# Kernel tuning notes

Measured on AMD Instinct MI355X. Metric: run time of the kernel, lower is better.

Reference implementation:

```python
import jax, jax.numpy as jnp
import numpy as np

B, C, H, W = 4, 256, 64, 64
G = 32          # GroupNorm groups
EPS = 1e-6


def setup_inputs() -> dict:
    key = jax.random.key(0)
    ks = jax.random.split(key, 6)
    inp = {
        "x": jax.random.normal(ks[0], (B, C, H, W), dtype=jnp.float32),
        "gamma": jnp.ones((C,), jnp.float32),
        "beta": jnp.zeros((C,), jnp.float32),
        "wq": jax.random.normal(ks[1], (C, C), jnp.float32) * 0.02,
        "bq": jnp.zeros((C,), jnp.float32),
        "wk": jax.random.normal(ks[2], (C, C), jnp.float32) * 0.02,
        "bk": jnp.zeros((C,), jnp.float32),
        "wv": jax.random.normal(ks[3], (C, C), jnp.float32) * 0.02,
        "bv": jnp.zeros((C,), jnp.float32),
        "wp": jax.random.normal(ks[4], (C, C), jnp.float32) * 0.02,
        "bp": jnp.zeros((C,), jnp.float32),
    }
    return inp


def _group_norm(x, gamma, beta):
    b, c, h, w = x.shape
    xs = x.reshape(b, G, c // G, h, w)
    mu = xs.mean(axis=(2, 3, 4), keepdims=True)
    var = xs.var(axis=(2, 3, 4), keepdims=True)  # biased, matches torch GroupNorm
    xn = ((xs - mu) * jax.lax.rsqrt(var + EPS)).reshape(b, c, h, w)
    return xn * gamma[None, :, None, None] + beta[None, :, None, None]


def _conv1x1(s, w, bias):
    # 1x1 conv == per-pixel channel matmul
    return jnp.einsum('oc,bchw->bohw', w, s) + bias[None, :, None, None]


def reference(x, gamma, beta, wq, bq, wk, bk, wv, bv, wp, bp):
    b, c, h, w = x.shape
    s = _group_norm(x, gamma, beta)
    q = _conv1x1(s, wq, bq).reshape(b, c, h * w)  # [B, C, N]
    k = _conv1x1(s, wk, bk).reshape(b, c, h * w)
    v = _conv1x1(s, wv, bv).reshape(b, c, h * w)
    # scores[b,i,j] = sum_c q[b,c,i] k[b,c,j], scaled by C^-1/2
    scores = jnp.einsum('bci,bcj->bij', q, k) * (c ** -0.5)
    attn = jax.nn.softmax(scores, axis=2)
    # h_[b,c,i] = sum_j v[b,c,j] attn[b,i,j]
    h_ = jnp.einsum('bij,bcj->bci', attn, v).reshape(b, c, h, w)
    h_ = _conv1x1(h_, wp, bp)
    return x + h_
```

## Files before the change

### kernel.cpp

```cpp
#include <hip/hip_runtime.h>

#define BB 4
#define CCH 256
#define NPIX 4096
#define EPS 1e-6f

typedef __attribute__((ext_vector_type(8))) short bf16x8;
typedef __attribute__((ext_vector_type(4))) float f32x4;
typedef __attribute__((ext_vector_type(16))) float f32x16;

__device__ __forceinline__ unsigned short f2bf(float f) {
    return (unsigned short)((__float_as_uint(f) + 0x8000u) >> 16);
}
__device__ __forceinline__ float bf2f(unsigned short h) {
    return __uint_as_float((unsigned)h << 16);
}
__device__ __forceinline__ void gl2lds16(const void* g, void* l) {
    __builtin_amdgcn_global_load_lds(
        (const __attribute__((address_space(1))) unsigned int*)g,
        (__attribute__((address_space(3))) unsigned int*)l, 16, 0, 0);
}
__device__ __forceinline__ unsigned int comb2(unsigned int u0, unsigned int u1,
                                              float f) {
    float lo = (bf2f((unsigned short)u0) + bf2f((unsigned short)u1)) * f;
    float hi = (bf2f((unsigned short)(u0 >> 16)) +
                bf2f((unsigned short)(u1 >> 16))) * f;
    return (unsigned int)f2bf(lo) | ((unsigned int)f2bf(hi) << 16);
}

__global__ __launch_bounds__(512) void gn_fused(
    const float* __restrict__ x, const float* __restrict__ gamma,
    const float* __restrict__ beta,
    const float* __restrict__ wq, const float* __restrict__ wk,
    const float* __restrict__ wv, const float* __restrict__ wp,
    unsigned short* __restrict__ sb, unsigned short* __restrict__ wb) {
    int bid = blockIdx.x;
    int t = threadIdx.x;
    if (bid >= 128) {
        int e = (bid - 128) * 512 + t;
        const float* srcs[4] = {wp, wq, wk, wv};
#pragma unroll
        for (int m = 0; m < 4; ++m) {
            float4 v = ((const float4*)srcs[m])[e];
            ushort4 hh;
            hh.x = f2bf(v.x); hh.y = f2bf(v.y);
            hh.z = f2bf(v.z); hh.w = f2bf(v.w);
            *(ushort4*)(wb + (size_t)m * 65536 + (size_t)e * 4) = hh;
        }
        return;
    }
    int b = bid >> 5, g = bid & 31;
    const float4* x4 = (const float4*)(x + (size_t)(b * CCH + g * 8) * NPIX);
    float s = 0.f, ss = 0.f;
    for (int e = t; e < 8192; e += 512) {
        float4 v = x4[e];
        s += v.x + v.y + v.z + v.w;
        ss += v.x * v.x + v.y * v.y + v.z * v.z + v.w * v.w;
    }
#pragma unroll
    for (int off = 1; off < 64; off <<= 1) {
        s += __shfl_xor(s, off);
        ss += __shfl_xor(ss, off);
    }
    __shared__ float ws[8], wss[8];
    int w = t >> 6, lane = t & 63;
    if (lane == 0) { ws[w] = s; wss[w] = ss; }
    __syncthreads();
    float S = 0.f, SS = 0.f;
#pragma unroll
    for (int i = 0; i < 8; ++i) { S += ws[i]; SS += wss[i]; }
    const float inv = 1.0f / (float)(8 * NPIX);
    float m = S * inv;
    float var = SS * inv - m * m;
    float rstd = rsqrtf(var + EPS);
    float scale[8], shift[8];
#pragma unroll
    for (int ci = 0; ci < 8; ++ci) {
        float ga = gamma[g * 8 + ci], be = beta[g * 8 + ci];
        scale[ci] = rstd * ga;
        shift[ci] = be - m * scale[ci];
    }
#pragma unroll 1
    for (int r = 0; r < 2; ++r) {
        int pq = r * 512 + t;
        __align__(16) unsigned short hh[4][8];
#pragma unroll
        for (int ci = 0; ci < 8; ++ci) {
            float4 v = x4[ci * 1024 + pq];
            hh[0][ci] = f2bf(v.x * scale[ci] + shift[ci]);
            hh[1][ci] = f2bf(v.y * scale[ci] + shift[ci]);
            hh[2][ci] = f2bf(v.z * scale[ci] + shift[ci]);
            hh[3][ci] = f2bf(v.w * scale[ci] + shift[ci]);
        }
        size_t base = ((size_t)(b * NPIX + pq * 4) << 8) + g * 8;
#pragma unroll
        for (int p = 0; p < 4; ++p)
            *(uint4*)(sb + base + (size_t)p * 256) = *(const uint4*)hh[p];
    }
}

__global__ __launch_bounds__(256) void qkv_mfma(
    const unsigned short* __restrict__ sb, const unsigned short* __restrict__ wb,
    const float* __restrict__ bq, const float* __restrict__ bk,
    const float* __restrict__ bv,
    unsigned short* __restrict__ qT, unsigned short* __restrict__ kT,
    unsigned short* __restrict__ vB) {
    __shared__ __align__(16) char lds[34816];
    const int tid = threadIdx.x, lane = tid & 63, w = tid >> 6;
    const int ln15 = lane & 15, q = lane >> 4;
    const int n0 = blockIdx.x * 128;
    const int co0 = blockIdx.y * 128;
    const int z = blockIdx.z;
    const unsigned short* wm = wb + (size_t)(z + 1) * 65536;
    const float* bias = (z == 0) ? bq : (z == 1) ? bk : bv;

    f32x4 acc[2][8];
#pragma unroll
    for (int i2 = 0; i2 < 2; ++i2)
#pragma unroll
        for (int nf = 0; nf < 8; ++nf) {
            acc[i2][nf][0] = 0.f; acc[i2][nf][1] = 0.f;
            acc[i2][nf][2] = 0.f; acc[i2][nf][3] = 0.f;
        }

#pragma unroll 1
    for (int kt = 0; kt < 4; ++kt) {
#pragma unroll
        for (int r = 0; r < 4; ++r) {
            int gch = r * 256 + tid;
            int row = gch >> 3, sidx = gch & 7;
            int cc = sidx ^ (row & 7);
            gl2lds16(sb + ((size_t)(n0 + row) << 8) + kt * 64 + cc * 8,
                     &lds[r * 4096 + w * 1024]);
            gl2lds16(wm + ((size_t)(co0 + row) << 8) + kt * 64 + cc * 8,
                     &lds[16384 + r * 4096 + w * 1024]);
        }
        __syncthreads();
#pragma unroll
        for (int kk = 0; kk < 2; ++kk) {
            int kc = kk * 4 + q;
            bf16x8 af[2], bf[8];
#pragma unroll
            for (int i2 = 0; i2 < 2; ++i2) {
                int row = w * 32 + i2 * 16 + ln15;
                af[i2] = *(const bf16x8*)&lds[row * 128 + ((kc ^ (row & 7)) << 4)];
            }
#pragma unroll
            for (int nf = 0; nf < 8; ++nf) {
                int row = nf * 16 + ln15;
                bf[nf] = *(const bf16x8*)&lds[16384 + row * 128 + ((kc ^ (row & 7)) << 4)];
            }
#pragma unroll
            for (int i2 = 0; i2 < 2; ++i2)
#pragma unroll
                for (int nf = 0; nf < 8; ++nf)
                    acc[i2][nf] = __builtin_amdgcn_mfma_f32_16x16x32_bf16(
                        af[i2], bf[nf], acc[i2][nf], 0, 0, 0);
        }
        __syncthreads();
    }

    float bias_l[8];
#pragma unroll
    for (int nf = 0; nf < 8; ++nf) bias_l[nf] = bias[co0 + nf * 16 + ln15];
    const float scl = (z == 0) ? 0.0625f : 1.0f;
    unsigned short* T = (unsigned short*)lds;
    if (z < 2) {
#pragma unroll
        for (int i2 = 0; i2 < 2; ++i2)
#pragma unroll
            for (int nf = 0; nf < 8; ++nf)
#pragma unroll
                for (int r = 0; r < 4; ++r) {
                    int n_l = w * 32 + i2 * 16 + q * 4 + r;
                    int co_l = nf * 16 + ln15;
                    T[n_l * 136 + co_l] = f2bf((acc[i2][nf][r] + bias_l[nf]) * scl);
                }
    } else {
#pragma unroll
        for (int i2 = 0; i2 < 2; ++i2)
#pragma unroll
            for (int nf = 0; nf < 8; ++nf)
#pragma unroll
                for (int r = 0; r < 4; ++r) {
                    int n_l = w * 32 + i2 * 16 + q * 4 + r;
                    int co_l = nf * 16 + ln15;
                    T[co_l * 136 + n_l] = f2bf(acc[i2][nf][r] + bias_l[nf]);
                }
    }
    __syncthreads();
    int row = tid >> 1, half = tid & 1;
    const uint4* src = (const uint4*)&T[row * 136 + half * 64];
    uint4* dst;
    if (z < 2) {
        unsigned short* qk = (z == 0) ? qT : kT;
        dst = (uint4*)(qk + ((size_t)(n0 + row) << 8) + co0 + half * 64);
    } else {
        int b2 = n0 >> 12, pix0 = n0 & 4095;
        dst = (uint4*)(vB + ((size_t)(b2 * CCH + co0 + row) << 12) + pix0 + half * 64);
    }
#pragma unroll
    for (int u = 0; u < 8; ++u) dst[u] = src[u];
}

__global__ __launch_bounds__(512, 1) void attn_mfma(
    const unsigned short* __restrict__ qT, const unsigned short* __restrict__ kT,
    const unsigned short* __restrict__ vB,
    unsigned short* __restrict__ pO, float* __restrict__ pml) {
    __shared__ __align__(16) char lds[147456];
    const int tid = threadIdx.x, lane = tid & 63, w = tid >> 6;
    const int l31 = lane & 31, lh = lane >> 5;
    const int bx = blockIdx.x;
    const int xk = bx & 7;
    const int b = xk >> 1, bjh = xk & 1;
    const int itile = bx >> 3;
    const int i0 = itile * 128;
    const int jbase = bjh * 2048;
    const size_t nb = (size_t)b * NPIX;
    const int iqb = (w >> 1) * 32;
    const int jh = w & 1, jwb = jh * 32;
    const int ipb = (w & 1) * 64;
    const int cqb = (w >> 1) * 64;

#pragma unroll
    for (int t = 0; t < 8; ++t) {
        int gch = (w * 8 + t) * 64 + lane;
        int row = gch >> 5, sc = gch & 31;
        int cc = sc ^ (row & 7);
        gl2lds16(qT + ((nb + i0 + row) << 8) + cc * 8, &lds[(w * 8 + t) * 1024]);
    }
    __syncthreads();
    bf16x8 qf[16];
    {
        int row = iqb + l31;
#pragma unroll
        for (int kc = 0; kc < 16; ++kc) {
            int sc = kc * 2 + lh;
            qf[kc] = *(const bf16x8*)&lds[row * 512 + ((sc ^ (row & 7)) << 4)];
        }
    }
    __syncthreads();

    f32x16 O[2][2];
#pragma unroll
    for (int ig = 0; ig < 2; ++ig)
#pragma unroll
        for (int cg = 0; cg < 2; ++cg)
#pragma unroll
            for (int r = 0; r < 16; ++r) O[ig][cg][r] = 0.f;
    float l_acc[16];
#pragma unroll
    for (int r = 0; r < 16; ++r) l_acc[r] = 0.f;

    {
        const int j0 = jbase;
#pragma unroll
        for (int t = 0; t < 4; ++t) {
            int gch = (w * 4 + t) * 64 + lane;
            int row = gch >> 5, sc = gch & 31;
            int cc = sc ^ (row & 7);
            gl2lds16(kT + ((nb + j0 + row) << 8) + cc * 8, &lds[(w * 4 + t) * 1024]);
        }
#pragma unroll
        for (int t = 0; t < 4; ++t) {
            int gch = (w * 4 + t) * 64 + lane;
            int c = gch >> 3, sv = gch & 7;
            int jc = sv ^ (c & 7);
            gl2lds16(vB + ((size_t)(b * CCH + c) << 12) + j0 + jc * 8,
                     &lds[65536 + (w * 4 + t) * 1024]);
        }
    }

#pragma unroll 1
    for (int jt = 0; jt < 32; ++jt) {
        const int kb_ = (jt & 1) * 32768;
        const int vb_ = 65536 + (jt & 1) * 32768;
        const int kbn = ((jt + 1) & 1) * 32768;
        const int vbn = 65536 + ((jt + 1) & 1) * 32768;

        asm volatile("s_waitcnt vmcnt(4)" ::: "memory");
        __builtin_amdgcn_s_barrier();

        f32x16 S0, S1;
#pragma unroll
        for (int r = 0; r < 16; ++r) { S0[r] = 0.f; S1[r] = 0.f; }
        __builtin_amdgcn_s_setprio(1);
        {
            int krow = jwb + l31;
            int ksw = kb_ + krow * 512;
#pragma unroll
            for (int kc = 0; kc < 8; ++kc) {
                int sc0 = (2 * kc) * 2 + lh;
                int sc1 = (2 * kc + 1) * 2 + lh;
                bf16x8 k0 = *(const bf16x8*)&lds[ksw + ((sc0 ^ (krow & 7)) << 4)];
                bf16x8 k1 = *(const bf16x8*)&lds[ksw + ((sc1 ^ (krow & 7)) << 4)];
                S0 = __builtin_amdgcn_mfma_f32_32x32x16_bf16(qf[2 * kc], k0, S0, 0, 0, 0);
                S1 = __builtin_amdgcn_mfma_f32_32x32x16_bf16(qf[2 * kc + 1], k1, S1, 0, 0, 0);
            }
        }
        __builtin_amdgcn_s_setprio(0);

        {
            int col = jwb + l31;
            int chs = (col >> 3) << 4;
            int cof = (col & 7) << 1;
#pragma unroll
            for (int r = 0; r < 16; ++r) {
                float p = __expf(S0[r] + S1[r]);
                l_acc[r] += p;
                int row = iqb + (r & 3) + 8 * (r >> 2) + 4 * lh;
                *(unsigned short*)&lds[131072 + row * 128 +
                    (chs ^ ((row & 7) << 4)) + cof] = f2bf(p);
            }
        }
        asm volatile("s_waitcnt lgkmcnt(0)" ::: "memory");
        __builtin_amdgcn_sched_barrier(0);
        asm volatile("s_waitcnt vmcnt(0)" ::: "memory");
        __builtin_amdgcn_s_barrier();

        if (jt < 31) {
            const int j0n = jbase + (jt + 1) * 64;
#pragma unroll
            for (int t = 0; t < 4; ++t) {
                int gch = (w * 4 + t) * 64 + lane;
                int row = gch >> 5, sc = gch & 31;
                int cc = sc ^ (row & 7);
                gl2lds16(kT + ((nb + j0n + row) << 8) + cc * 8,
                         &lds[kbn + (w * 4 + t) * 1024]);
            }
        }

        __builtin_amdgcn_s_setprio(1);
        {
            int pr0 = ipb + l31, pr1 = ipb + 32 + l31;
            int vc0 = cqb + l31, vc1 = cqb + 32 + l31;
#pragma unroll
            for (int kc = 0; kc < 4; ++kc) {
                int pc = kc * 2 + lh;
                bf16x8 pf0 = *(const bf16x8*)&lds[131072 + pr0 * 128 + ((pc ^ (pr0 & 7)) << 4)];
                bf16x8 pf1 = *(const bf16x8*)&lds[131072 + pr1 * 128 + ((pc ^ (pr1 & 7)) << 4)];
                bf16x8 vf0 = *(const bf16x8*)&lds[vb_ + vc0 * 128 + ((pc ^ (vc0 & 7)) << 4)];
                bf16x8 vf1 = *(const bf16x8*)&lds[vb_ + vc1 * 128 + ((pc ^ (vc1 & 7)) << 4)];
                O[0][0] = __builtin_amdgcn_mfma_f32_32x32x16_bf16(pf0, vf0, O[0][0], 0, 0, 0);
                O[0][1] = __builtin_amdgcn_mfma_f32_32x32x16_bf16(pf0, vf1, O[0][1], 0, 0, 0);
                O[1][0] = __builtin_amdgcn_mfma_f32_32x32x16_bf16(pf1, vf0, O[1][0], 0, 0, 0);
                O[1][1] = __builtin_amdgcn_mfma_f32_32x32x16_bf16(pf1, vf1, O[1][1], 0, 0, 0);
            }
        }
        __builtin_amdgcn_s_setprio(0);

        if (jt < 31) {
            const int j0n = jbase + (jt + 1) * 64;
#pragma unroll
            for (int t = 0; t < 4; ++t) {
                int gch = (w * 4 + t) * 64 + lane;
                int c = gch >> 3, sv = gch & 7;
                int jc = sv ^ (c & 7);
                gl2lds16(vB + ((size_t)(b * CCH + c) << 12) + j0n + jc * 8,
                         &lds[vbn + (w * 4 + t) * 1024]);
            }
        }
    }

    size_t pbase = (size_t)bx * (128 * 256);
#pragma unroll
    for (int ig = 0; ig < 2; ++ig)
#pragma unroll
        for (int cg = 0; cg < 2; ++cg)
#pragma unroll
            for (int r = 0; r < 16; ++r) {
                int i = ipb + ig * 32 + (r & 3) + 8 * (r >> 2) + 4 * lh;
                int c = cqb + cg * 32 + l31;
                pO[pbase + i * 256 + c] = f2bf(O[ig][cg][r]);
            }
#pragma unroll
    for (int r = 0; r < 16; ++r) {
        float l = l_acc[r];
        l += __shfl_xor(l, 1);
        l += __shfl_xor(l, 2);
        l += __shfl_xor(l, 4);
        l += __shfl_xor(l, 8);
        l += __shfl_xor(l, 16);
        if (l31 == 0) {
            int row = iqb + (r & 3) + 8 * (r >> 2) + 4 * lh;
            pml[bx * 256 + jh * 128 + row] = l;
        }
    }
}

__global__ __launch_bounds__(256) void proj_mfma(
    const unsigned short* __restrict__ pO, const float* __restrict__ pml,
    const unsigned short* __restrict__ wb, const float* __restrict__ bp,
    const float* __restrict__ x, float* __restrict__ out) {
    __shared__ __align__(16) char lds[35328];
    float* fs = (float*)&lds[34816];
    const int tid = threadIdx.x, lane = tid & 63, w = tid >> 6;
    const int ln15 = lane & 15, q = lane >> 4;
    const int n0 = blockIdx.x * 128;
    const int co0 = blockIdx.y * 128;

    if (tid < 128) {
        int n = n0 + tid;
        int bb = n >> 12, pix = n & 4095, it = pix >> 7, ii = pix & 127;
        int base = (it * 8 + bb * 2) * 256 + ii;
        float l = pml[base] + pml[base + 128] + pml[base + 256] + pml[base + 384];
        fs[tid] = 1.0f / l;
    }
    __syncthreads();

    f32x4 acc[2][8];
#pragma unroll
    for (int i2 = 0; i2 < 2; ++i2)
#pragma unroll
        for (int nf = 0; nf < 8; ++nf) {
            acc[i2][nf][0] = 0.f; acc[i2][nf][1] = 0.f;
            acc[i2][nf][2] = 0.f; acc[i2][nf][3] = 0.f;
        }

#pragma unroll 1
    for (int kt = 0; kt < 4; ++kt) {
#pragma unroll
        for (int r = 0; r < 4; ++r) {
            int gch = r * 256 + tid;
            int row = gch >> 3, sidx = gch & 7;
            int cc = sidx ^ (row & 7);
            gl2lds16(wb + ((size_t)(co0 + row) << 8) + kt * 64 + cc * 8,
                     &lds[16384 + r * 4096 + w * 1024]);
        }
#pragma unroll
        for (int r = 0; r < 4; ++r) {
            int gch = r * 256 + tid;
            int row = gch >> 3, sidx = gch & 7;
            int cc = sidx ^ (row & 7);
            int c = kt * 64 + cc * 8;
            int n = n0 + row;
            int bb = n >> 12, pix = n & 4095, it = pix >> 7, ii = pix & 127;
            size_t pb = (size_t)(it * 8 + bb * 2) * 32768 + (size_t)ii * 256 + c;
            uint4 a0 = *(const uint4*)&pO[pb];
            uint4 a1 = *(const uint4*)&pO[pb + 32768];
            float f = fs[row];
            uint4 o;
            o.x = comb2(a0.x, a1.x, f);
            o.y = comb2(a0.y, a1.y, f);
            o.z = comb2(a0.z, a1.z, f);
            o.w = comb2(a0.w, a1.w, f);
            *(uint4*)&lds[r * 4096 + w * 1024 + lane * 16] = o;
        }
        __syncthreads();
#pragma unroll
        for (int kk = 0; kk < 2; ++kk) {
            int kc = kk * 4 + q;
            bf16x8 af[2], bf[8];
#pragma unroll
            for (int i2 = 0; i2 < 2; ++i2) {
                int row = w * 32 + i2 * 16 + ln15;
                af[i2] = *(const bf16x8*)&lds[row * 128 + ((kc ^ (row & 7)) << 4)];
            }
#pragma unroll
            for (int nf = 0; nf < 8; ++nf) {
                int row = nf * 16 + ln15;
                bf[nf] = *(const bf16x8*)&lds[16384 + row * 128 + ((kc ^ (row & 7)) << 4)];
            }
#pragma unroll
            for (int i2 = 0; i2 < 2; ++i2)
#pragma unroll
                for (int nf = 0; nf < 8; ++nf)
                    acc[i2][nf] = __builtin_amdgcn_mfma_f32_16x16x32_bf16(
                        af[i2], bf[nf], acc[i2][nf], 0, 0, 0);
        }
        __syncthreads();
    }

    unsigned short* T = (unsigned short*)lds;
#pragma unroll
    for (int i2 = 0; i2 < 2; ++i2)
#pragma unroll
        for (int nf = 0; nf < 8; ++nf)
#pragma unroll
            for (int r = 0; r < 4; ++r) {
                int n_l = w * 32 + i2 * 16 + q * 4 + r;
                int co_l = nf * 16 + ln15;
                T[co_l * 136 + n_l] = f2bf(acc[i2][nf][r]);
            }
    __syncthreads();
    int row = tid >> 1, half = tid & 1;
    int b2 = n0 >> 12, pix0 = n0 & 4095;
    float br = bp[co0 + row];
    size_t gidx = (((size_t)(b2 * CCH + co0 + row)) << 12) + pix0 + half * 64;
    const unsigned short* trow = &T[row * 136 + half * 64];
#pragma unroll
    for (int u = 0; u < 16; ++u) {
        float4 xv = *(const float4*)&x[gidx + u * 4];
        ushort4 tv = *(const ushort4*)&trow[u * 4];
        float4 o;
        o.x = xv.x + br + bf2f(tv.x);
        o.y = xv.y + br + bf2f(tv.y);
        o.z = xv.z + br + bf2f(tv.z);
        o.w = xv.w + br + bf2f(tv.w);
        *(float4*)&out[gidx + u * 4] = o;
    }
}

extern "C" void kernel_launch(void* const* d_in, const int* in_sizes, int n_in,
                              void* d_out, int out_size, void* d_ws, size_t ws_size,
                              hipStream_t stream) {
    const float* x     = (const float*)d_in[0];
    const float* gamma = (const float*)d_in[1];
    const float* beta  = (const float*)d_in[2];
    const float* wq    = (const float*)d_in[3];
    const float* bq    = (const float*)d_in[4];
    const float* wk    = (const float*)d_in[5];
    const float* bk    = (const float*)d_in[6];
    const float* wv    = (const float*)d_in[7];
    const float* bv    = (const float*)d_in[8];
    const float* wp    = (const float*)d_in[9];
    const float* bp    = (const float*)d_in[10];
    float* out = (float*)d_out;

    char* p = (char*)d_ws;
    unsigned short* sb  = (unsigned short*)p; p += 8388608;
    unsigned short* wb  = (unsigned short*)p; p += 524288;
    unsigned short* pO  = (unsigned short*)p; p += 16777216;
    float*          pml = (float*)p;          p += 262144;
    unsigned short* qT  = (unsigned short*)p; p += 8388608;
    unsigned short* kT  = (unsigned short*)p; p += 8388608;
    unsigned short* vB  = (unsigned short*)p;

    gn_fused<<<160, 512, 0, stream>>>(x, gamma, beta, wq, wk, wv, wp, sb, wb);
    qkv_mfma<<<dim3(128, 2, 3), 256, 0, stream>>>(sb, wb, bq, bk, bv, qT, kT, vB);
    attn_mfma<<<256, 512, 0, stream>>>(qT, kT, vB, pO, pml);
    proj_mfma<<<dim3(128, 2), 256, 0, stream>>>(pO, pml, wb, bp, x, out);
}
```

Measured before the change: 209.8 us.

## Load V fragments directly from global into registers, dropping the LDS V buffers

The attention kernel stops staging V tiles through double-buffered LDS. Each wave now reads its own V fragments from global memory into registers at the start of every key tile, and those reads overlap with the QK MFMA work. The next K-tile prefetch is moved to the top of the loop, and one barrier and the explicit vmcnt(0) wait are removed. This cuts LDS footprint and LDS read traffic and shortens the synchronisation chain. In exchange, global V reads are duplicated across the wave pairs that share the same channel slice, global-load latency is exposed inside each iteration, and the code now depends on compiler-inserted waits to ensure the async K loads have landed.

```diff
diff --git a/kernel.cpp b/kernel.cpp
--- a/kernel.cpp
+++ b/kernel.cpp
@@ -207,7 +207,7 @@
     const unsigned short* __restrict__ qT, const unsigned short* __restrict__ kT,
     const unsigned short* __restrict__ vB,
     unsigned short* __restrict__ pO, float* __restrict__ pml) {
-    __shared__ __align__(16) char lds[147456];
+    __shared__ __align__(16) char lds[81920];
     const int tid = threadIdx.x, lane = tid & 63, w = tid >> 6;
     const int l31 = lane & 31, lh = lane >> 5;
     const int bx = blockIdx.x;
@@ -221,6 +221,8 @@
     const int jh = w & 1, jwb = jh * 32;
     const int ipb = (w & 1) * 64;
     const int cqb = (w >> 1) * 64;
+    const unsigned short* vrow0 = vB + ((size_t)(b * CCH + cqb + l31) << 12);
+    const unsigned short* vrow1 = vrow0 + ((size_t)32 << 12);
 
 #pragma unroll
     for (int t = 0; t < 8; ++t) {
@@ -261,25 +263,36 @@
             int cc = sc ^ (row & 7);
             gl2lds16(kT + ((nb + j0 + row) << 8) + cc * 8, &lds[(w * 4 + t) * 1024]);
         }
-#pragma unroll
-        for (int t = 0; t < 4; ++t) {
-            int gch = (w * 4 + t) * 64 + lane;
-            int c = gch >> 3, sv = gch & 7;
-            int jc = sv ^ (c & 7);
-            gl2lds16(vB + ((size_t)(b * CCH + c) << 12) + j0 + jc * 8,
-                     &lds[65536 + (w * 4 + t) * 1024]);
-        }
-    }
+    }
+    __syncthreads();
 
 #pragma unroll 1
     for (int jt = 0; jt < 32; ++jt) {
         const int kb_ = (jt & 1) * 32768;
-        const int vb_ = 65536 + (jt & 1) * 32768;
         const int kbn = ((jt + 1) & 1) * 32768;
-        const int vbn = 65536 + ((jt + 1) & 1) * 32768;
-
-        asm volatile("s_waitcnt vmcnt(4)" ::: "memory");
-        __builtin_amdgcn_s_barrier();
+        const int j0 = jbase + jt * 64;
+
+        if (jt) __builtin_amdgcn_s_barrier();
+
+        if (jt < 31) {
+            const int j0n = j0 + 64;
+#pragma unroll
+            for (int t = 0; t < 4; ++t) {
+                int gch = (w * 4 + t) * 64 + lane;
+                int row = gch >> 5, sc = gch & 31;
+                int cc = sc ^ (row & 7);
+                gl2lds16(kT + ((nb + j0n + row) << 8) + cc * 8,
+                         &lds[kbn + (w * 4 + t) * 1024]);
+            }
+        }
+
+        bf16x8 vg[4][2];
+#pragma unroll
+        for (int kc = 0; kc < 4; ++kc) {
+            int joff = j0 + kc * 16 + lh * 8;
+            vg[kc][0] = *(const bf16x8*)(vrow0 + joff);
+            vg[kc][1] = *(const bf16x8*)(vrow1 + joff);
+        }
 
         f32x16 S0, S1;
 #pragma unroll
@@ -309,57 +322,29 @@
                 float p = __expf(S0[r] + S1[r]);
                 l_acc[r] += p;
                 int row = iqb + (r & 3) + 8 * (r >> 2) + 4 * lh;
-                *(unsigned short*)&lds[131072 + row * 128 +
+                *(unsigned short*)&lds[65536 + row * 128 +
                     (chs ^ ((row & 7) << 4)) + cof] = f2bf(p);
             }
         }
         asm volatile("s_waitcnt lgkmcnt(0)" ::: "memory");
         __builtin_amdgcn_sched_barrier(0);
-        asm volatile("s_waitcnt vmcnt(0)" ::: "memory");
         __builtin_amdgcn_s_barrier();
-
-        if (jt < 31) {
-            const int j0n = jbase + (jt + 1) * 64;
-#pragma unroll
-            for (int t = 0; t < 4; ++t) {
-                int gch = (w * 4 + t) * 64 + lane;
-                int row = gch >> 5, sc = gch & 31;
-                int cc = sc ^ (row & 7);
-                gl2lds16(kT + ((nb + j0n + row) << 8) + cc * 8,
-                         &lds[kbn + (w * 4 + t) * 1024]);
-            }
-        }
 
         __builtin_amdgcn_s_setprio(1);
         {
             int pr0 = ipb + l31, pr1 = ipb + 32 + l31;
-            int vc0 = cqb + l31, vc1 = cqb + 32 + l31;
 #pragma unroll
             for (int kc = 0; kc < 4; ++kc) {
                 int pc = kc * 2 + lh;
-                bf16x8 pf0 = *(const bf16x8*)&lds[131072 + pr0 * 128 + ((pc ^ (pr0 & 7)) << 4)];
-                bf16x8 pf1 = *(const bf16x8*)&lds[131072 + pr1 * 128 + ((pc ^ (pr1 & 7)) << 4)];
-                bf16x8 vf0 = *(const bf16x8*)&lds[vb_ + vc0 * 128 + ((pc ^ (vc0 & 7)) << 4)];
-                bf16x8 vf1 = *(const bf16x8*)&lds[vb_ + vc1 * 128 + ((pc ^ (vc1 & 7)) << 4)];
-                O[0][0] = __builtin_amdgcn_mfma_f32_32x32x16_bf16(pf0, vf0, O[0][0], 0, 0, 0);
-                O[0][1] = __builtin_amdgcn_mfma_f32_32x32x16_bf16(pf0, vf1, O[0][1], 0, 0, 0);
-                O[1][0] = __builtin_amdgcn_mfma_f32_32x32x16_bf16(pf1, vf0, O[1][0], 0, 0, 0);
-                O[1][1] = __builtin_amdgcn_mfma_f32_32x32x16_bf16(pf1, vf1, O[1][1], 0, 0, 0);
+                bf16x8 pf0 = *(const bf16x8*)&lds[65536 + pr0 * 128 + ((pc ^ (pr0 & 7)) << 4)];
+                bf16x8 pf1 = *(const bf16x8*)&lds[65536 + pr1 * 128 + ((pc ^ (pr1 & 7)) << 4)];
+                O[0][0] = __builtin_amdgcn_mfma_f32_32x32x16_bf16(pf0, vg[kc][0], O[0][0], 0, 0, 0);
+                O[0][1] = __builtin_amdgcn_mfma_f32_32x32x16_bf16(pf0, vg[kc][1], O[0][1], 0, 0, 0);
+                O[1][0] = __builtin_amdgcn_mfma_f32_32x32x16_bf16(pf1, vg[kc][0], O[1][0], 0, 0, 0);
+                O[1][1] = __builtin_amdgcn_mfma_f32_32x32x16_bf16(pf1, vg[kc][1], O[1][1], 0, 0, 0);
             }
         }
         __builtin_amdgcn_s_setprio(0);
-
-        if (jt < 31) {
-            const int j0n = jbase + (jt + 1) * 64;
-#pragma unroll
-            for (int t = 0; t < 4; ++t) {
-                int gch = (w * 4 + t) * 64 + lane;
-                int c = gch >> 3, sv = gch & 7;
-                int jc = sv ^ (c & 7);
-                gl2lds16(vB + ((size_t)(b * CCH + c) << 12) + j0n + jc * 8,
-                         &lds[vbn + (w * 4 + t) * 1024]);
-            }
-        }
     }
 
     size_t pbase = (size_t)bx * (128 * 256);
```

New measurement: 309.8 us. 47.7% more time.
